# Kernel optimization log

Measured on AMD Instinct MI355X. Metric: run time of the kernel, lower is better.

Reference implementation:

```python
import jax, jax.numpy as jnp
import numpy as np

B, S, D, N = 8, 2048, 1024, 1024
RMIN, RMAX = 0.9, 0.999
MAX_PHASE = 6.2831853
EPS = 1e-5


def _ln(v):
    # LayerNorm without affine params (elementwise_affine=False)
    mu = jnp.mean(v, axis=-1, keepdims=True)
    var = jnp.var(v, axis=-1, keepdims=True)
    return (v - mu) * jax.lax.rsqrt(var + EPS)


def setup_inputs() -> dict:
    key = jax.random.key(0)
    ks = jax.random.split(key, 12)
    x = jax.random.normal(ks[0], (B, S, D), dtype=jnp.float32)
    hidden_re = jnp.zeros((B, N), dtype=jnp.float32)
    hidden_im = jnp.zeros((B, N), dtype=jnp.float32)
    # LRU ring initialization (Orvieto et al. 2023)
    u1 = jax.random.uniform(ks[1], (N,), dtype=jnp.float32)
    u2 = jax.random.uniform(ks[2], (N,), dtype=jnp.float32)
    nu_log = jnp.log(-0.5 * jnp.log(u1 * (RMAX**2 - RMIN**2) + RMIN**2))
    theta_log = jnp.log(MAX_PHASE * u2)
    B_re = jax.random.normal(ks[3], (N, D), dtype=jnp.float32) / np.sqrt(2 * D)
    B_im = jax.random.normal(ks[4], (N, D), dtype=jnp.float32) / np.sqrt(2 * D)
    C_re = jax.random.normal(ks[5], (N, N), dtype=jnp.float32) / np.sqrt(N)
    C_im = jax.random.normal(ks[6], (N, N), dtype=jnp.float32) / np.sqrt(N)
    D_skip = jax.random.normal(ks[7], (N, D), dtype=jnp.float32) / np.sqrt(D)
    W_gate = jax.random.normal(ks[8], (N, D), dtype=jnp.float32) / np.sqrt(D)  # gating_proj
    W_con = jax.random.normal(ks[9], (D, N), dtype=jnp.float32) / np.sqrt(N)   # contract
    return {"x": x, "hidden_re": hidden_re, "hidden_im": hidden_im,
            "nu_log": nu_log, "theta_log": theta_log,
            "B_re": B_re, "B_im": B_im, "C_re": C_re, "C_im": C_im,
            "D_skip": D_skip, "W_gate": W_gate, "W_con": W_con}


def reference(x, hidden_re, hidden_im, nu_log, theta_log,
              B_re, B_im, C_re, C_im, D_skip, W_gate, W_con):
    residual = x
    # diagonal complex transition lambda and input normalizer gamma
    mag = jnp.exp(-jnp.exp(nu_log))                 # |lambda|, [N]
    phase = jnp.exp(theta_log)
    lam_re = mag * jnp.cos(phase)
    lam_im = mag * jnp.sin(phase)
    gamma = jnp.sqrt(1.0 - mag * mag)               # sqrt(1-|lambda|^2)
    # input projection (complex), pre-scaled by gamma: [B,S,N]
    u_re = jnp.einsum("bsd,nd->bsn", x, B_re) * gamma
    u_im = jnp.einsum("bsd,nd->bsn", x, B_im) * gamma
    # sequential linear recurrence h_t = lambda * h_{t-1} + u_t (complex)
    def step(h, u):
        h_re, h_im = h
        ur, ui = u
        nr = lam_re * h_re - lam_im * h_im + ur
        ni = lam_re * h_im + lam_im * h_re + ui
        return (nr, ni), (nr, ni)
    (hf_re, hf_im), (hs_re, hs_im) = jax.lax.scan(
        step, (hidden_re, hidden_im),
        (jnp.swapaxes(u_re, 0, 1), jnp.swapaxes(u_im, 0, 1)))  # time-major [S,B,N]
    hs_re = jnp.swapaxes(hs_re, 0, 1)  # [B,S,N]
    hs_im = jnp.swapaxes(hs_im, 0, 1)
    # y = Re(C h) + D x
    y = (jnp.einsum("bsn,mn->bsm", hs_re, C_re)
         - jnp.einsum("bsn,mn->bsm", hs_im, C_im)
         + jnp.einsum("bsd,md->bsm", x, D_skip))
    # gated norm / MLP fusion
    y = _ln(y)                                              # rnn_post_norm
    gate = jax.nn.gelu(_ln(jnp.einsum("bsd,nd->bsn", residual, W_gate)), approximate=False)
    y = y * gate
    y = jax.nn.gelu(_ln(y), approximate=False)              # contract_norm + activation
    out = jnp.einsum("bsn,dn->bsd", y, W_con)               # contract
    return (out, hf_re, hf_im)
```

## Files before the change

### kernel.cpp

```cpp
#include <hip/hip_runtime.h>
#include <math.h>

#define Bsz 8
#define Ssz 2048
#define Dsz 1024
#define Nsz 1024
#define CHUNKS 64
#define CLEN 32
#define Msz (Bsz * Ssz)
#define Ksz 1024

typedef unsigned short u16;
typedef __attribute__((ext_vector_type(8))) short short8;
typedef __attribute__((ext_vector_type(4))) float floatx4;

__device__ __forceinline__ float b2f(u16 u) {
    unsigned v = ((unsigned)u) << 16; float f; __builtin_memcpy(&f, &v, 4); return f;
}
__device__ __forceinline__ u16 f2b(float f) {
    unsigned u; __builtin_memcpy(&u, &f, 4);
    unsigned r = u + 0x7fffu + ((u >> 16) & 1u);
    return (u16)(r >> 16);
}

struct CvtJobs {
    const float* src[8];
    u16* dst[8];
    int n4[8];
    float scale[8];
    int blk_start[9];
};

__global__ __launch_bounds__(256)
void cvt_multi(CvtJobs J) {
    int b = blockIdx.x;
    int j = 0;
    #pragma unroll
    for (int t = 0; t < 7; ++t) if (b >= J.blk_start[t + 1]) j = t + 1;
    int i = (b - J.blk_start[j]) * 256 + threadIdx.x;
    if (i < J.n4[j]) {
        float4 v = ((const float4*)J.src[j])[i];
        float s = J.scale[j];
        ushort4 o;
        o.x = f2b(v.x * s); o.y = f2b(v.y * s);
        o.z = f2b(v.z * s); o.w = f2b(v.w * s);
        ((ushort4*)J.dst[j])[i] = o;
    }
}

__global__ void lam_setup(const float* __restrict__ nu_log, const float* __restrict__ theta_log,
                          float* lam_re, float* lam_im, float* gam,
                          float* lamL_re, float* lamL_im) {
    int n = blockIdx.x * 256 + threadIdx.x;
    if (n >= Nsz) return;
    float mag = expf(-expf(nu_log[n]));
    float ph  = expf(theta_log[n]);
    float lr = mag * cosf(ph), li = mag * sinf(ph);
    lam_re[n] = lr; lam_im[n] = li;
    gam[n] = sqrtf(fmaxf(1.0f - mag * mag, 0.0f));
    float ar = lr, ai = li;
    #pragma unroll
    for (int i = 0; i < 5; ++i) { float nr = ar*ar - ai*ai; float ni = 2.0f*ar*ai; ar = nr; ai = ni; }
    lamL_re[n] = ar; lamL_im[n] = ai;
}

#define BM 128
#define BN 128
#define BK 32
#define KITER 32

struct GemmJob {
    const u16* A0; const u16* W0;
    const u16* A1; const u16* W1;
    const u16* A2; const u16* W2;
    int P;
    float* outF;
    u16*   outB;
    const float* colscale;
};
struct GemmBatch { GemmJob j[3]; };

__global__ __launch_bounds__(256, 3)
void gemm_bt(GemmBatch batch) {
    const GemmJob job = batch.j[blockIdx.z];
    __shared__ u16 As[2][BM * BK];
    __shared__ u16 Ws[2][BN * BK];
    const int tid  = threadIdx.x;
    const int wave = tid >> 6, lane = tid & 63;
    const int bm = blockIdx.x, bn = blockIdx.y;
    const int wm = (wave >> 1) * 64, wn = (wave & 1) * 64;

    floatx4 acc[4][4];
    #pragma unroll
    for (int i = 0; i < 4; ++i)
        #pragma unroll
        for (int j = 0; j < 4; ++j) acc[i][j] = (floatx4){0.f, 0.f, 0.f, 0.f};

    const u16* Aps[3] = { job.A0, job.A1, job.A2 };
    const u16* Wps[3] = { job.W0, job.W1, job.W2 };
    const int TOT = job.P * KITER;

    const int srow = wave * 32 + (lane >> 2);
    const int scol = ((lane & 3) ^ ((lane >> 3) & 3)) * 8;
    const size_t sAoff = (size_t)(bm * BM + srow) * Ksz + scol;
    const size_t sWoff = (size_t)(bn * BN + srow) * Ksz + scol;
    const int frow = lane & 15;
    const int fk   = (((lane >> 4) ^ ((frow >> 1) & 3))) * 8;

    {
        const u16* gA = Aps[0] + sAoff;
        const u16* gW = Wps[0] + sWoff;
        #pragma unroll
        for (int jj = 0; jj < 2; ++jj) {
            u16* lA = &As[0][(wave * 32 + jj * 16) * BK];
            u16* lW = &Ws[0][(wave * 32 + jj * 16) * BK];
            __builtin_amdgcn_global_load_lds((const __attribute__((address_space(1))) void*)(gA + (size_t)(jj * 16) * Ksz),
                                             (__attribute__((address_space(3))) void*)lA, 16, 0, 0);
            __builtin_amdgcn_global_load_lds((const __attribute__((address_space(1))) void*)(gW + (size_t)(jj * 16) * Ksz),
                                             (__attribute__((address_space(3))) void*)lW, 16, 0, 0);
        }
    }

    for (int i = 0; i < TOT; ++i) {
        const int cur = i & 1;
        __syncthreads();
        if (i + 1 < TOT) {
            const int ni = i + 1;
            const int p = ni >> 5;
            const int koff = (ni & 31) * BK;
            const u16* gA = Aps[p] + sAoff + koff;
            const u16* gW = Wps[p] + sWoff + koff;
            const int nb = cur ^ 1;
            #pragma unroll
            for (int jj = 0; jj < 2; ++jj) {
                u16* lA = &As[nb][(wave * 32 + jj * 16) * BK];
                u16* lW = &Ws[nb][(wave * 32 + jj * 16) * BK];
                __builtin_amdgcn_global_load_lds((const __attribute__((address_space(1))) void*)(gA + (size_t)(jj * 16) * Ksz),
                                                 (__attribute__((address_space(3))) void*)lA, 16, 0, 0);
                __builtin_amdgcn_global_load_lds((const __attribute__((address_space(1))) void*)(gW + (size_t)(jj * 16) * Ksz),
                                                 (__attribute__((address_space(3))) void*)lW, 16, 0, 0);
            }
        }
        short8 af[4], wf[4];
        #pragma unroll
        for (int t = 0; t < 4; ++t)
            af[t] = *(const short8*)(&As[cur][(wm + t * 16 + frow) * BK + fk]);
        #pragma unroll
        for (int t = 0; t < 4; ++t)
            wf[t] = *(const short8*)(&Ws[cur][(wn + t * 16 + frow) * BK + fk]);
        #pragma unroll
        for (int mi = 0; mi < 4; ++mi)
            #pragma unroll
            for (int ni2 = 0; ni2 < 4; ++ni2)
                acc[mi][ni2] = __builtin_amdgcn_mfma_f32_16x16x32_bf16(af[mi], wf[ni2], acc[mi][ni2], 0, 0, 0);
    }

    const int rgrp = lane >> 4;
    const int ccol = lane & 15;
    #pragma unroll
    for (int mi = 0; mi < 4; ++mi) {
        #pragma unroll
        for (int r = 0; r < 4; ++r) {
            int row = bm * BM + wm + mi * 16 + rgrp * 4 + r;
            #pragma unroll
            for (int ni = 0; ni < 4; ++ni) {
                int col = bn * BN + wn + ni * 16 + ccol;
                float v = acc[mi][ni][r];
                if (job.colscale) v *= job.colscale[col];
                size_t idx = (size_t)row * Nsz + col;
                if (job.outF) job.outF[idx] = v;
                else          job.outB[idx] = f2b(v);
            }
        }
    }
}

__global__ void scan_phase1(const u16* __restrict__ u_re, const u16* __restrict__ u_im,
                            const float* __restrict__ lam_re, const float* __restrict__ lam_im,
                            float* __restrict__ carry_re, float* __restrict__ carry_im) {
    int n = threadIdx.x * 4;
    int c = blockIdx.x, b = blockIdx.y;
    float4 lr = *(const float4*)(lam_re + n);
    float4 li = *(const float4*)(lam_im + n);
    size_t base = ((size_t)b * Ssz + (size_t)c * CLEN) * Nsz + n;
    float hr[4] = {0.f, 0.f, 0.f, 0.f}, hi[4] = {0.f, 0.f, 0.f, 0.f};
    const float* lrp = (const float*)&lr; const float* lip = (const float*)&li;
    #pragma unroll
    for (int t = 0; t < CLEN; ++t) {
        ushort4 urv = *(const ushort4*)(u_re + base + (size_t)t * Nsz);
        ushort4 uiv = *(const ushort4*)(u_im + base + (size_t)t * Nsz);
        float ur[4] = { b2f(urv.x), b2f(urv.y), b2f(urv.z), b2f(urv.w) };
        float ui[4] = { b2f(uiv.x), b2f(uiv.y), b2f(uiv.z), b2f(uiv.w) };
        #pragma unroll
        for (int q = 0; q < 4; ++q) {
            float nr = fmaf(lrp[q], hr[q], fmaf(-lip[q], hi[q], ur[q]));
            float ni = fmaf(lrp[q], hi[q], fmaf( lip[q], hr[q], ui[q]));
            hr[q] = nr; hi[q] = ni;
        }
    }
    size_t ci = ((size_t)b * CHUNKS + c) * Nsz + n;
    *(float4*)(carry_re + ci) = (float4){hr[0], hr[1], hr[2], hr[3]};
    *(float4*)(carry_im + ci) = (float4){hi[0], hi[1], hi[2], hi[3]};
}

__global__ void scan_phase2(const float* __restrict__ carry_re, const float* __restrict__ carry_im,
                            const float* __restrict__ lamL_re, const float* __restrict__ lamL_im,
                            const float* __restrict__ hid_re, const float* __restrict__ hid_im,
                            float* __restrict__ entry_re, float* __restrict__ entry_im,
                            float* __restrict__ out_base) {
    int n = blockIdx.x * 256 + threadIdx.x;
    int b = blockIdx.y;
    float Lr = lamL_re[n], Li = lamL_im[n];
    float Hr = hid_re[b * Nsz + n], Hi = hid_im[b * Nsz + n];
    for (int c = 0; c < CHUNKS; ++c) {
        size_t ci = ((size_t)b * CHUNKS + c) * Nsz + n;
        entry_re[ci] = Hr; entry_im[ci] = Hi;
        float cr = carry_re[ci], cim = carry_im[ci];
        float nr = fmaf(Lr, Hr, fmaf(-Li, Hi, cr));
        float ni = fmaf(Lr, Hi, fmaf( Li, Hr, cim));
        Hr = nr; Hi = ni;
    }
    out_base[(size_t)16777216 + (size_t)b * Nsz + n] = Hr;
    out_base[(size_t)16777216 + 8192 + (size_t)b * Nsz + n] = Hi;
}

__global__ void scan_phase3(const u16* __restrict__ u_re, const u16* __restrict__ u_im,
                            const float* __restrict__ lam_re, const float* __restrict__ lam_im,
                            const float* __restrict__ entry_re, const float* __restrict__ entry_im,
                            u16* __restrict__ hs_re, u16* __restrict__ hs_im) {
    int n = threadIdx.x * 4;
    int c = blockIdx.x, b = blockIdx.y;
    float4 lr = *(const float4*)(lam_re + n);
    float4 li = *(const float4*)(lam_im + n);
    const float* lrp = (const float*)&lr; const float* lip = (const float*)&li;
    size_t ci = ((size_t)b * CHUNKS + c) * Nsz + n;
    float4 er = *(const float4*)(entry_re + ci);
    float4 ei = *(const float4*)(entry_im + ci);
    float hr[4] = {er.x, er.y, er.z, er.w}, hi[4] = {ei.x, ei.y, ei.z, ei.w};
    size_t base = ((size_t)b * Ssz + (size_t)c * CLEN) * Nsz + n;
    #pragma unroll
    for (int t = 0; t < CLEN; ++t) {
        ushort4 urv = *(const ushort4*)(u_re + base + (size_t)t * Nsz);
        ushort4 uiv = *(const ushort4*)(u_im + base + (size_t)t * Nsz);
        float ur[4] = { b2f(urv.x), b2f(urv.y), b2f(urv.z), b2f(urv.w) };
        float ui[4] = { b2f(uiv.x), b2f(uiv.y), b2f(uiv.z), b2f(uiv.w) };
        ushort4 orv, oiv;
        u16* orp = (u16*)&orv; u16* oip = (u16*)&oiv;
        #pragma unroll
        for (int q = 0; q < 4; ++q) {
            float nr = fmaf(lrp[q], hr[q], fmaf(-lip[q], hi[q], ur[q]));
            float ni = fmaf(lrp[q], hi[q], fmaf( lip[q], hr[q], ui[q]));
            hr[q] = nr; hi[q] = ni;
            orp[q] = f2b(nr); oip[q] = f2b(ni);
        }
        *(ushort4*)(hs_re + base + (size_t)t * Nsz) = orv;
        *(ushort4*)(hs_im + base + (size_t)t * Nsz) = oiv;
    }
}

__device__ __forceinline__ float waveReduce(float v) {
    #pragma unroll
    for (int off = 32; off > 0; off >>= 1) v += __shfl_down(v, off, 64);
    return v;
}
__device__ __forceinline__ float gelu_exact(float x) {
    return 0.5f * x * (1.0f + erff(x * 0.70710678118654752f));
}

__global__ __launch_bounds__(256)
void fuse_ln(const u16* __restrict__ y_raw, const u16* __restrict__ gate_pre, u16* __restrict__ y3) {
    int row = blockIdx.x;
    int tid = threadIdx.x;
    int wave = tid >> 6, lane = tid & 63;
    size_t base = (size_t)row * Nsz + tid * 4;
    ushort4 yv = *(const ushort4*)(y_raw + base);
    ushort4 gv = *(const ushort4*)(gate_pre + base);
    float y[4] = { b2f(yv.x), b2f(yv.y), b2f(yv.z), b2f(yv.w) };
    float g[4] = { b2f(gv.x), b2f(gv.y), b2f(gv.z), b2f(gv.w) };

    float sy = 0.f, sy2 = 0.f, sg = 0.f, sg2 = 0.f;
    #pragma unroll
    for (int i = 0; i < 4; ++i) {
        sy += y[i]; sy2 += y[i] * y[i];
        sg += g[i]; sg2 += g[i] * g[i];
    }
    __shared__ float sh[16];
    sy = waveReduce(sy); sy2 = waveReduce(sy2);
    sg = waveReduce(sg); sg2 = waveReduce(sg2);
    if (lane == 0) { sh[wave] = sy; sh[wave + 4] = sy2; sh[wave + 8] = sg; sh[wave + 12] = sg2; }
    __syncthreads();
    sy  = sh[0] + sh[1] + sh[2] + sh[3];
    sy2 = sh[4] + sh[5] + sh[6] + sh[7];
    sg  = sh[8] + sh[9] + sh[10] + sh[11];
    sg2 = sh[12] + sh[13] + sh[14] + sh[15];
    const float inv = 1.0f / (float)Nsz;
    float muy = sy * inv, vary = sy2 * inv - muy * muy, ry = rsqrtf(vary + 1e-5f);
    float mug = sg * inv, varg = sg2 * inv - mug * mug, rg = rsqrtf(varg + 1e-5f);

    float y2[4]; float s2 = 0.f, s22 = 0.f;
    #pragma unroll
    for (int i = 0; i < 4; ++i) {
        float ly = (y[i] - muy) * ry;
        float lg = (g[i] - mug) * rg;
        float t = ly * gelu_exact(lg);
        y2[i] = t; s2 += t; s22 += t * t;
    }
    s2 = waveReduce(s2); s22 = waveReduce(s22);
    __syncthreads();
    if (lane == 0) { sh[wave] = s2; sh[wave + 4] = s22; }
    __syncthreads();
    s2  = sh[0] + sh[1] + sh[2] + sh[3];
    s22 = sh[4] + sh[5] + sh[6] + sh[7];
    float mu2 = s2 * inv, var2 = s22 * inv - mu2 * mu2, r2 = rsqrtf(var2 + 1e-5f);
    ushort4 ov;
    ov.x = f2b(gelu_exact((y2[0] - mu2) * r2));
    ov.y = f2b(gelu_exact((y2[1] - mu2) * r2));
    ov.z = f2b(gelu_exact((y2[2] - mu2) * r2));
    ov.w = f2b(gelu_exact((y2[3] - mu2) * r2));
    *(ushort4*)(y3 + base) = ov;
}

extern "C" void kernel_launch(void* const* d_in, const int* in_sizes, int n_in,
                              void* d_out, int out_size, void* d_ws, size_t ws_size,
                              hipStream_t stream) {
    const float* x         = (const float*)d_in[0];
    const float* hid_re    = (const float*)d_in[1];
    const float* hid_im    = (const float*)d_in[2];
    const float* nu_log    = (const float*)d_in[3];
    const float* theta_log = (const float*)d_in[4];
    const float* B_re      = (const float*)d_in[5];
    const float* B_im      = (const float*)d_in[6];
    const float* C_re      = (const float*)d_in[7];
    const float* C_im      = (const float*)d_in[8];
    const float* D_skip    = (const float*)d_in[9];
    const float* W_gate    = (const float*)d_in[10];
    const float* W_con     = (const float*)d_in[11];
    float* out = (float*)d_out;

    char* ws = (char*)d_ws;
    const size_t MB = 1ull << 20;
    u16* wBre  = (u16*)(ws + 0 * MB);
    u16* wBim  = (u16*)(ws + 2 * MB);
    u16* wCre  = (u16*)(ws + 4 * MB);
    u16* wCimN = (u16*)(ws + 6 * MB);
    u16* wDsk  = (u16*)(ws + 8 * MB);
    u16* wWg   = (u16*)(ws + 10 * MB);
    u16* wWc   = (u16*)(ws + 12 * MB);
    float* lam_re = (float*)(ws + 14 * MB);
    float* lam_im = lam_re + 1024;
    float* gam    = lam_re + 2048;
    float* lamLre = lam_re + 3072;
    float* lamLim = lam_re + 4096;
    u16* xb    = (u16*)(ws + 16 * MB);
    u16* u_re  = (u16*)(ws + 48 * MB);
    u16* u_im  = (u16*)(ws + 80 * MB);
    u16* gate  = (u16*)(ws + 112 * MB);
    u16* hs_re = (u16*)(ws + 144 * MB);
    u16* hs_im = (u16*)(ws + 176 * MB);
    float* carry_re = (float*)(ws + 208 * MB);
    float* carry_im = (float*)(ws + 210 * MB);
    float* entry_re = (float*)(ws + 212 * MB);
    float* entry_im = (float*)(ws + 214 * MB);
    u16* y_raw = u_re;
    u16* y3    = u_im;

    CvtJobs J = {};
    const int WQ = (Nsz * Dsz) / 4;
    const int WB = WQ / 256;
    J.src[0] = x;      J.dst[0] = xb;    J.n4[0] = (Msz * Dsz) / 4; J.scale[0] = 1.0f;
    J.src[1] = B_re;   J.dst[1] = wBre;  J.n4[1] = WQ; J.scale[1] = 1.0f;
    J.src[2] = B_im;   J.dst[2] = wBim;  J.n4[2] = WQ; J.scale[2] = 1.0f;
    J.src[3] = C_re;   J.dst[3] = wCre;  J.n4[3] = WQ; J.scale[3] = 1.0f;
    J.src[4] = C_im;   J.dst[4] = wCimN; J.n4[4] = WQ; J.scale[4] = -1.0f;
    J.src[5] = D_skip; J.dst[5] = wDsk;  J.n4[5] = WQ; J.scale[5] = 1.0f;
    J.src[6] = W_gate; J.dst[6] = wWg;   J.n4[6] = WQ; J.scale[6] = 1.0f;
    J.src[7] = W_con;  J.dst[7] = wWc;   J.n4[7] = WQ; J.scale[7] = 1.0f;
    J.blk_start[0] = 0;
    J.blk_start[1] = 16384;
    for (int t = 2; t <= 8; ++t) J.blk_start[t] = J.blk_start[t - 1] + WB;
    cvt_multi<<<J.blk_start[8], 256, 0, stream>>>(J);
    lam_setup<<<4, 256, 0, stream>>>(nu_log, theta_log, lam_re, lam_im, gam, lamLre, lamLim);

    GemmBatch b1 = {};
    b1.j[0] = { xb, wBre, nullptr, nullptr, nullptr, nullptr, 1, nullptr, u_re, gam };
    b1.j[1] = { xb, wBim, nullptr, nullptr, nullptr, nullptr, 1, nullptr, u_im, gam };
    b1.j[2] = { xb, wWg,  nullptr, nullptr, nullptr, nullptr, 1, nullptr, gate, nullptr };
    gemm_bt<<<dim3(Msz / BM, Nsz / BN, 3), 256, 0, stream>>>(b1);

    scan_phase1<<<dim3(CHUNKS, Bsz), 256, 0, stream>>>(u_re, u_im, lam_re, lam_im, carry_re, carry_im);
    scan_phase2<<<dim3(Nsz / 256, Bsz), 256, 0, stream>>>(carry_re, carry_im, lamLre, lamLim,
                                                          hid_re, hid_im, entry_re, entry_im, out);
    scan_phase3<<<dim3(CHUNKS, Bsz), 256, 0, stream>>>(u_re, u_im, lam_re, lam_im,
                                                       entry_re, entry_im, hs_re, hs_im);

    GemmBatch b2 = {};
    b2.j[0] = { hs_re, wCre, hs_im, wCimN, xb, wDsk, 3, nullptr, y_raw, nullptr };
    gemm_bt<<<dim3(Msz / BM, Nsz / BN, 1), 256, 0, stream>>>(b2);

    fuse_ln<<<Msz, 256, 0, stream>>>(y_raw, gate, y3);

    GemmBatch b3 = {};
    b3.j[0] = { y3, wWc, nullptr, nullptr, nullptr, nullptr, 1, out, nullptr, nullptr };
    gemm_bt<<<dim3(Msz / BM, Dsz / BN, 1), 256, 0, stream>>>(b3);

    (void)in_sizes; (void)n_in; (void)out_size; (void)ws_size;
}
```

Baseline: 523.6 us.

## Enlarge GEMM tile to 256x128x64 and drop LDS double buffering

Grows the bf16 GEMM block tile to 256x128 with a K step of 64, so each wave computes a 128x64 sub-tile with 32 accumulators. The LDS double buffer is replaced by one buffer with load, sync and compute steps, and the swizzle is reworked for the wider K. Larger tiles raise arithmetic intensity per global load and halve the number of blocks. In exchange the register footprint grows, occupancy falls to 2 blocks, and load latency is no longer overlapped with MFMA work. The host launch grid must also match the new BM, which is not shown here.

Measured after the change: 482.3 us. -7.9%, faster.

```diff
diff --git a/kernel.cpp b/kernel.cpp
--- a/kernel.cpp
+++ b/kernel.cpp
@@ -64,10 +64,10 @@
     lamL_re[n] = ar; lamL_im[n] = ai;
 }
 
-#define BM 128
+#define BM 256
 #define BN 128
-#define BK 32
-#define KITER 32
+#define BK 64
+#define KITER 16
 
 struct GemmJob {
     const u16* A0; const u16* W0;
@@ -80,19 +80,20 @@
 };
 struct GemmBatch { GemmJob j[3]; };
 
-__global__ __launch_bounds__(256, 3)
+__global__ __launch_bounds__(256, 2)
 void gemm_bt(GemmBatch batch) {
     const GemmJob job = batch.j[blockIdx.z];
-    __shared__ u16 As[2][BM * BK];
-    __shared__ u16 Ws[2][BN * BK];
+    __shared__ u16 As[BM * BK];
+    __shared__ u16 Ws[BN * BK];
     const int tid  = threadIdx.x;
     const int wave = tid >> 6, lane = tid & 63;
     const int bm = blockIdx.x, bn = blockIdx.y;
-    const int wm = (wave >> 1) * 64, wn = (wave & 1) * 64;
-
-    floatx4 acc[4][4];
-    #pragma unroll
-    for (int i = 0; i < 4; ++i)
+    const int wm = (wave >> 1) * 128;
+    const int wn = (wave & 1) * 64;
+
+    floatx4 acc[8][4];
+    #pragma unroll
+    for (int i = 0; i < 8; ++i)
         #pragma unroll
         for (int j = 0; j < 4; ++j) acc[i][j] = (floatx4){0.f, 0.f, 0.f, 0.f};
 
@@ -100,65 +101,57 @@
     const u16* Wps[3] = { job.W0, job.W1, job.W2 };
     const int TOT = job.P * KITER;
 
-    const int srow = wave * 32 + (lane >> 2);
-    const int scol = ((lane & 3) ^ ((lane >> 3) & 3)) * 8;
-    const size_t sAoff = (size_t)(bm * BM + srow) * Ksz + scol;
-    const size_t sWoff = (size_t)(bn * BN + srow) * Ksz + scol;
+    const int srow8 = lane >> 3;
+    const int scol  = ((lane & 7) ^ srow8) * 8;
+    const size_t sAbase = (size_t)(bm * BM + wave * 64 + srow8) * Ksz + scol;
+    const size_t sWbase = (size_t)(bn * BN + wave * 32 + srow8) * Ksz + scol;
     const int frow = lane & 15;
-    const int fk   = (((lane >> 4) ^ ((frow >> 1) & 3))) * 8;
-
-    {
-        const u16* gA = Aps[0] + sAoff;
-        const u16* gW = Wps[0] + sWoff;
-        #pragma unroll
-        for (int jj = 0; jj < 2; ++jj) {
-            u16* lA = &As[0][(wave * 32 + jj * 16) * BK];
-            u16* lW = &Ws[0][(wave * 32 + jj * 16) * BK];
-            __builtin_amdgcn_global_load_lds((const __attribute__((address_space(1))) void*)(gA + (size_t)(jj * 16) * Ksz),
-                                             (__attribute__((address_space(3))) void*)lA, 16, 0, 0);
-            __builtin_amdgcn_global_load_lds((const __attribute__((address_space(1))) void*)(gW + (size_t)(jj * 16) * Ksz),
-                                             (__attribute__((address_space(3))) void*)lW, 16, 0, 0);
-        }
-    }
+    const int fq   = lane >> 4;
+    const int fsw  = frow & 7;
 
     for (int i = 0; i < TOT; ++i) {
-        const int cur = i & 1;
+        const int p    = i >> 4;
+        const int koff = (i & 15) * BK;
+        const u16* Ap = Aps[p];
+        const u16* Wp = Wps[p];
         __syncthreads();
-        if (i + 1 < TOT) {
-            const int ni = i + 1;
-            const int p = ni >> 5;
-            const int koff = (ni & 31) * BK;
-            const u16* gA = Aps[p] + sAoff + koff;
-            const u16* gW = Wps[p] + sWoff + koff;
-            const int nb = cur ^ 1;
+        #pragma unroll
+        for (int jj = 0; jj < 8; ++jj) {
+            const u16* g = Ap + sAbase + (size_t)(jj * 8) * Ksz + koff;
+            u16* l = &As[(wave * 64 + jj * 8) * BK];
+            __builtin_amdgcn_global_load_lds((const __attribute__((address_space(1))) void*)g,
+                                             (__attribute__((address_space(3))) void*)l, 16, 0, 0);
+        }
+        #pragma unroll
+        for (int jj = 0; jj < 4; ++jj) {
+            const u16* g = Wp + sWbase + (size_t)(jj * 8) * Ksz + koff;
+            u16* l = &Ws[(wave * 32 + jj * 8) * BK];
+            __builtin_amdgcn_global_load_lds((const __attribute__((address_space(1))) void*)g,
+                                             (__attribute__((address_space(3))) void*)l, 16, 0, 0);
+        }
+        __syncthreads();
+        #pragma unroll
+        for (int h = 0; h < 2; ++h) {
+            const int ca = ((h << 2) | fq) ^ fsw;
+            short8 af[8], wf[4];
             #pragma unroll
-            for (int jj = 0; jj < 2; ++jj) {
-                u16* lA = &As[nb][(wave * 32 + jj * 16) * BK];
-                u16* lW = &Ws[nb][(wave * 32 + jj * 16) * BK];
-                __builtin_amdgcn_global_load_lds((const __attribute__((address_space(1))) void*)(gA + (size_t)(jj * 16) * Ksz),
-                                                 (__attribute__((address_space(3))) void*)lA, 16, 0, 0);
-                __builtin_amdgcn_global_load_lds((const __attribute__((address_space(1))) void*)(gW + (size_t)(jj * 16) * Ksz),
-                                                 (__attribute__((address_space(3))) void*)lW, 16, 0, 0);
-            }
-        }
-        short8 af[4], wf[4];
-        #pragma unroll
-        for (int t = 0; t < 4; ++t)
-            af[t] = *(const short8*)(&As[cur][(wm + t * 16 + frow) * BK + fk]);
-        #pragma unroll
-        for (int t = 0; t < 4; ++t)
-            wf[t] = *(const short8*)(&Ws[cur][(wn + t * 16 + frow) * BK + fk]);
-        #pragma unroll
-        for (int mi = 0; mi < 4; ++mi)
+            for (int t = 0; t < 8; ++t)
+                af[t] = *(const short8*)(&As[(wm + t * 16 + frow) * BK + ca * 8]);
             #pragma unroll
-            for (int ni2 = 0; ni2 < 4; ++ni2)
-                acc[mi][ni2] = __builtin_amdgcn_mfma_f32_16x16x32_bf16(af[mi], wf[ni2], acc[mi][ni2], 0, 0, 0);
+            for (int t = 0; t < 4; ++t)
+                wf[t] = *(const short8*)(&Ws[(wn + t * 16 + frow) * BK + ca * 8]);
+            #pragma unroll
+            for (int mi = 0; mi < 8; ++mi)
+                #pragma unroll
+                for (int ni = 0; ni < 4; ++ni)
+                    acc[mi][ni] = __builtin_amdgcn_mfma_f32_16x16x32_bf16(af[mi], wf[ni], acc[mi][ni], 0, 0, 0);
+        }
     }
 
     const int rgrp = lane >> 4;
     const int ccol = lane & 15;
     #pragma unroll
-    for (int mi = 0; mi < 4; ++mi) {
+    for (int mi = 0; mi < 8; ++mi) {
         #pragma unroll
         for (int r = 0; r < 4; ++r) {
             int row = bm * BM + wm + mi * 16 + rgrp * 4 + r;
```

## Replace double-buffered GEMM with multi-slab rounds of larger K per barrier

Applied to the files above, without the earlier changes.

The double-buffered BK=32 GEMM main loop is replaced by a templated kernel that loads several K-slabs (or several A/W operand pairs) into shared memory per round, then runs all their MFMAs between two barriers. The aim is fewer barriers per unit of compute and more MFMA work per synchronisation. The cost is that global loads are no longer overlapped with compute, since loads and compute alternate within each round. Shared memory per block grows and the occupancy hint drops from 3 to 2 blocks per CU.

Measured after the change: 553.9 us. +5.8%, slower.

```diff
diff --git a/kernel.cpp b/kernel.cpp
--- a/kernel.cpp
+++ b/kernel.cpp
@@ -64,27 +64,23 @@
     lamL_re[n] = ar; lamL_im[n] = ai;
 }
 
-#define BM 128
-#define BN 128
 #define BK 32
-#define KITER 32
-
-struct GemmJob {
-    const u16* A0; const u16* W0;
-    const u16* A1; const u16* W1;
-    const u16* A2; const u16* W2;
-    int P;
+
+struct MJob {
+    const u16* A[4]; const u16* W[4];
+    int kstep, kpair, rounds;
     float* outF;
     u16*   outB;
     const float* colscale;
 };
-struct GemmBatch { GemmJob j[3]; };
-
-__global__ __launch_bounds__(256, 3)
-void gemm_bt(GemmBatch batch) {
-    const GemmJob job = batch.j[blockIdx.z];
-    __shared__ u16 As[2][BM * BK];
-    __shared__ u16 Ws[2][BN * BK];
+struct MBatch { MJob j[3]; };
+
+template<int PAIRS>
+__global__ __launch_bounds__(256, 2)
+void gemm_multi(MBatch batch) {
+    const MJob job = batch.j[blockIdx.z];
+    __shared__ u16 As[PAIRS][128 * BK];
+    __shared__ u16 Ws[PAIRS][128 * BK];
     const int tid  = threadIdx.x;
     const int wave = tid >> 6, lane = tid & 63;
     const int bm = blockIdx.x, bn = blockIdx.y;
@@ -96,63 +92,46 @@
         #pragma unroll
         for (int j = 0; j < 4; ++j) acc[i][j] = (floatx4){0.f, 0.f, 0.f, 0.f};
 
-    const u16* Aps[3] = { job.A0, job.A1, job.A2 };
-    const u16* Wps[3] = { job.W0, job.W1, job.W2 };
-    const int TOT = job.P * KITER;
-
     const int srow = wave * 32 + (lane >> 2);
     const int scol = ((lane & 3) ^ ((lane >> 3) & 3)) * 8;
-    const size_t sAoff = (size_t)(bm * BM + srow) * Ksz + scol;
-    const size_t sWoff = (size_t)(bn * BN + srow) * Ksz + scol;
+    const size_t aoff = (size_t)(bm * 128 + srow) * Ksz + scol;
+    const size_t woff = (size_t)(bn * 128 + srow) * Ksz + scol;
     const int frow = lane & 15;
     const int fk   = (((lane >> 4) ^ ((frow >> 1) & 3))) * 8;
 
-    {
-        const u16* gA = Aps[0] + sAoff;
-        const u16* gW = Wps[0] + sWoff;
-        #pragma unroll
-        for (int jj = 0; jj < 2; ++jj) {
-            u16* lA = &As[0][(wave * 32 + jj * 16) * BK];
-            u16* lW = &Ws[0][(wave * 32 + jj * 16) * BK];
-            __builtin_amdgcn_global_load_lds((const __attribute__((address_space(1))) void*)(gA + (size_t)(jj * 16) * Ksz),
-                                             (__attribute__((address_space(3))) void*)lA, 16, 0, 0);
-            __builtin_amdgcn_global_load_lds((const __attribute__((address_space(1))) void*)(gW + (size_t)(jj * 16) * Ksz),
-                                             (__attribute__((address_space(3))) void*)lW, 16, 0, 0);
-        }
-    }
-
-    for (int i = 0; i < TOT; ++i) {
-        const int cur = i & 1;
+    for (int r = 0; r < job.rounds; ++r) {
         __syncthreads();
-        if (i + 1 < TOT) {
-            const int ni = i + 1;
-            const int p = ni >> 5;
-            const int koff = (ni & 31) * BK;
-            const u16* gA = Aps[p] + sAoff + koff;
-            const u16* gW = Wps[p] + sWoff + koff;
-            const int nb = cur ^ 1;
+        #pragma unroll
+        for (int p = 0; p < PAIRS; ++p) {
+            const int ko = r * job.kstep + p * job.kpair;
+            const u16* gA = job.A[p] + aoff + ko;
+            const u16* gW = job.W[p] + woff + ko;
             #pragma unroll
             for (int jj = 0; jj < 2; ++jj) {
-                u16* lA = &As[nb][(wave * 32 + jj * 16) * BK];
-                u16* lW = &Ws[nb][(wave * 32 + jj * 16) * BK];
+                u16* lA = &As[p][(wave * 32 + jj * 16) * BK];
+                u16* lW = &Ws[p][(wave * 32 + jj * 16) * BK];
                 __builtin_amdgcn_global_load_lds((const __attribute__((address_space(1))) void*)(gA + (size_t)(jj * 16) * Ksz),
                                                  (__attribute__((address_space(3))) void*)lA, 16, 0, 0);
                 __builtin_amdgcn_global_load_lds((const __attribute__((address_space(1))) void*)(gW + (size_t)(jj * 16) * Ksz),
                                                  (__attribute__((address_space(3))) void*)lW, 16, 0, 0);
             }
         }
-        short8 af[4], wf[4];
-        #pragma unroll
-        for (int t = 0; t < 4; ++t)
-            af[t] = *(const short8*)(&As[cur][(wm + t * 16 + frow) * BK + fk]);
-        #pragma unroll
-        for (int t = 0; t < 4; ++t)
-            wf[t] = *(const short8*)(&Ws[cur][(wn + t * 16 + frow) * BK + fk]);
-        #pragma unroll
-        for (int mi = 0; mi < 4; ++mi)
-            #pragma unroll
-            for (int ni2 = 0; ni2 < 4; ++ni2)
-                acc[mi][ni2] = __builtin_amdgcn_mfma_f32_16x16x32_bf16(af[mi], wf[ni2], acc[mi][ni2], 0, 0, 0);
+        __syncthreads();
+        #pragma unroll
+        for (int p = 0; p < PAIRS; ++p) {
+            short8 af[4], wf[4];
+            #pragma unroll
+            for (int t = 0; t < 4; ++t)
+                af[t] = *(const short8*)(&As[p][(wm + t * 16 + frow) * BK + fk]);
+            #pragma unroll
+            for (int t = 0; t < 4; ++t)
+                wf[t] = *(const short8*)(&Ws[p][(wn + t * 16 + frow) * BK + fk]);
+            #pragma unroll
+            for (int mi = 0; mi < 4; ++mi)
+                #pragma unroll
+                for (int ni = 0; ni < 4; ++ni)
+                    acc[mi][ni] = __builtin_amdgcn_mfma_f32_16x16x32_bf16(af[mi], wf[ni], acc[mi][ni], 0, 0, 0);
+        }
     }
 
     const int rgrp = lane >> 4;
@@ -161,10 +140,10 @@
     for (int mi = 0; mi < 4; ++mi) {
         #pragma unroll
         for (int r = 0; r < 4; ++r) {
-            int row = bm * BM + wm + mi * 16 + rgrp * 4 + r;
+            int row = bm * 128 + wm + mi * 16 + rgrp * 4 + r;
             #pragma unroll
             for (int ni = 0; ni < 4; ++ni) {
-                int col = bn * BN + wn + ni * 16 + ccol;
+                int col = bn * 128 + wn + ni * 16 + ccol;
                 float v = acc[mi][ni][r];
                 if (job.colscale) v *= job.colscale[col];
                 size_t idx = (size_t)row * Nsz + col;
@@ -381,11 +360,16 @@
     cvt_multi<<<J.blk_start[8], 256, 0, stream>>>(J);
     lam_setup<<<4, 256, 0, stream>>>(nu_log, theta_log, lam_re, lam_im, gam, lamLre, lamLim);
 
-    GemmBatch b1 = {};
-    b1.j[0] = { xb, wBre, nullptr, nullptr, nullptr, nullptr, 1, nullptr, u_re, gam };
-    b1.j[1] = { xb, wBim, nullptr, nullptr, nullptr, nullptr, 1, nullptr, u_im, gam };
-    b1.j[2] = { xb, wWg,  nullptr, nullptr, nullptr, nullptr, 1, nullptr, gate, nullptr };
-    gemm_bt<<<dim3(Msz / BM, Nsz / BN, 3), 256, 0, stream>>>(b1);
+    MBatch mb1 = {};
+    u16* outs1[3] = { u_re, u_im, gate };
+    const u16* ws1[3] = { wBre, wBim, wWg };
+    const float* cs1[3] = { gam, gam, nullptr };
+    for (int z = 0; z < 3; ++z) {
+        for (int p = 0; p < 4; ++p) { mb1.j[z].A[p] = xb; mb1.j[z].W[p] = ws1[z]; }
+        mb1.j[z].kstep = 128; mb1.j[z].kpair = 32; mb1.j[z].rounds = 8;
+        mb1.j[z].outF = nullptr; mb1.j[z].outB = outs1[z]; mb1.j[z].colscale = cs1[z];
+    }
+    gemm_multi<4><<<dim3(Msz / 128, Nsz / 128, 3), 256, 0, stream>>>(mb1);
 
     scan_phase1<<<dim3(CHUNKS, Bsz), 256, 0, stream>>>(u_re, u_im, lam_re, lam_im, carry_re, carry_im);
     scan_phase2<<<dim3(Nsz / 256, Bsz), 256, 0, stream>>>(carry_re, carry_im, lamLre, lamLim,
@@ -393,15 +377,21 @@
     scan_phase3<<<dim3(CHUNKS, Bsz), 256, 0, stream>>>(u_re, u_im, lam_re, lam_im,
                                                        entry_re, entry_im, hs_re, hs_im);
 
-    GemmBatch b2 = {};
-    b2.j[0] = { hs_re, wCre, hs_im, wCimN, xb, wDsk, 3, nullptr, y_raw, nullptr };
-    gemm_bt<<<dim3(Msz / BM, Nsz / BN, 1), 256, 0, stream>>>(b2);
+    MBatch mb2 = {};
+    mb2.j[0].A[0] = hs_re; mb2.j[0].W[0] = wCre;
+    mb2.j[0].A[1] = hs_im; mb2.j[0].W[1] = wCimN;
+    mb2.j[0].A[2] = xb;    mb2.j[0].W[2] = wDsk;
+    mb2.j[0].kstep = 32; mb2.j[0].kpair = 0; mb2.j[0].rounds = 32;
+    mb2.j[0].outF = nullptr; mb2.j[0].outB = y_raw; mb2.j[0].colscale = nullptr;
+    gemm_multi<3><<<dim3(Msz / 128, Nsz / 128, 1), 256, 0, stream>>>(mb2);
 
     fuse_ln<<<Msz, 256, 0, stream>>>(y_raw, gate, y3);
 
-    GemmBatch b3 = {};
-    b3.j[0] = { y3, wWc, nullptr, nullptr, nullptr, nullptr, 1, out, nullptr, nullptr };
-    gemm_bt<<<dim3(Msz / BM, Dsz / BN, 1), 256, 0, stream>>>(b3);
+    MBatch mb3 = {};
+    for (int p = 0; p < 4; ++p) { mb3.j[0].A[p] = y3; mb3.j[0].W[p] = wWc; }
+    mb3.j[0].kstep = 128; mb3.j[0].kpair = 32; mb3.j[0].rounds = 8;
+    mb3.j[0].outF = out; mb3.j[0].outB = nullptr; mb3.j[0].colscale = nullptr;
+    gemm_multi<4><<<dim3(Msz / 128, Dsz / 128, 1), 256, 0, stream>>>(mb3);
 
     (void)in_sizes; (void)n_in; (void)out_size; (void)ws_size;
 }
```
